# Kernel tuning notes

Hardware: AMD Instinct MI355X
Metric: run time of the kernel (lower is better)

The kernel has to match this reference:

```python
import jax, jax.numpy as jnp
import numpy as np

H = 1024
LENGTH = 48
N = 2048


def setup_inputs() -> dict:
    key = jax.random.key(0)
    k1, k2, k3, k4 = jax.random.split(key, 4)
    s = 1.0 / np.sqrt(H)  # torch LSTMCell init: U(-1/sqrt(H), 1/sqrt(H))
    h_in = jax.random.normal(k1, (N, H), dtype=jnp.float32)
    W_hh = jax.random.uniform(k2, (4 * H, H), minval=-s, maxval=s, dtype=jnp.float32)
    b_ih = jax.random.uniform(k3, (4 * H,), minval=-s, maxval=s, dtype=jnp.float32)
    b_hh = jax.random.uniform(k4, (4 * H,), minval=-s, maxval=s, dtype=jnp.float32)
    return {"h_in": h_in, "W_hh": W_hh, "b_ih": b_ih, "b_hh": b_hh}


def reference(h_in, W_hh, b_ih, b_hh):
    # LSTMCell with input_size=0: gates depend only on hidden state.
    # torch gate order: i, f, g, o.
    Hd = h_in.shape[1]
    bias = b_ih + b_hh
    c0 = jnp.zeros_like(h_in)

    def step(carry, _):
        h, c = carry
        z = h @ W_hh.T + bias  # (N, 4H)
        i = jax.nn.sigmoid(z[:, :Hd])
        f = jax.nn.sigmoid(z[:, Hd:2 * Hd])
        g = jnp.tanh(z[:, 2 * Hd:3 * Hd])
        o = jax.nn.sigmoid(z[:, 3 * Hd:])
        c_new = f * c + i * g
        h_new = o * jnp.tanh(c_new)
        return (h_new, c_new), h_new

    _, hs = jax.lax.scan(step, (h_in, c0), None, length=LENGTH)  # (L, N, H)
    return jnp.transpose(hs, (1, 2, 0))  # (N, H, L) matching torch.stack(axis=-1)
```

## Files before the change

kernel.cpp:

```cpp
#include <hip/hip_runtime.h>
#include <hip/hip_bf16.h>

#define Hdim 1024
#define Nb   2048
#define Lsteps 48

typedef unsigned short ushort_t;
typedef short bf16x8 __attribute__((ext_vector_type(8)));
typedef float f32x4 __attribute__((ext_vector_type(4)));

typedef __attribute__((address_space(3))) unsigned int lds_u32;
typedef const __attribute__((address_space(1))) unsigned int glb_u32;

__device__ __forceinline__ void gll16(const void* g, void* l) {
    __builtin_amdgcn_global_load_lds((glb_u32*)g, (lds_u32*)l, 16, 0, 0);
}

__device__ __forceinline__ ushort_t f2bf(float x) {
    unsigned u = __builtin_bit_cast(unsigned, x);
    unsigned r = u + 0x7fffu + ((u >> 16) & 1u);
    return (ushort_t)(r >> 16);
}

__device__ __forceinline__ float frcp(float x) { return __builtin_amdgcn_rcpf(x); }

__device__ __forceinline__ float fsigmoid(float x) {
    return frcp(1.0f + __expf(-x));
}
__device__ __forceinline__ float ftanh(float x) {
    float xm = fminf(fmaxf(x, -15.0f), 15.0f);
    float e = __expf(2.0f * xm);
    return (e - 1.0f) * frcp(e + 1.0f);
}

__device__ __forceinline__ f32x4 mfma16(bf16x8 a, bf16x8 b, f32x4 c) {
    return __builtin_amdgcn_mfma_f32_16x16x32_bf16(a, b, c, 0, 0, 0);
}

#define VMCNT8   asm volatile("s_waitcnt vmcnt(8)" ::: "memory")
#define VMCNT0   asm volatile("s_waitcnt vmcnt(0)" ::: "memory")
#define LGKMCNT0 asm volatile("s_waitcnt lgkmcnt(0)" ::: "memory")

__global__ __launch_bounds__(256) void prep_w(const float* __restrict__ W,
                                              ushort_t* __restrict__ Wb) {
    int i = blockIdx.x * 256 + threadIdx.x;
    Wb[i] = f2bf(W[i]);
}

__global__ __launch_bounds__(256) void prep_h(const float* __restrict__ h_in,
                                              ushort_t* __restrict__ h0,
                                              const float* __restrict__ b_ih,
                                              const float* __restrict__ b_hh,
                                              float* __restrict__ bias) {
    int i = blockIdx.x * 256 + threadIdx.x;
    h0[i] = f2bf(h_in[i]);
    if (i < 4 * Hdim) bias[i] = b_ih[i] + b_hh[i];
}

__global__ __launch_bounds__(256) void lstm_step(
    const ushort_t* __restrict__ hsrc,
    ushort_t* __restrict__ hdst,
    const ushort_t* __restrict__ Wb,
    const float* __restrict__ bias,
    float* __restrict__ cst,
    float* __restrict__ tmp)
{
    __shared__ __align__(16) ushort_t As[2][128 * 64];
    __shared__ __align__(16) ushort_t Bs[2][128 * 64];

    const int tid  = threadIdx.x;
    const int lane = tid & 63;
    const int wid  = tid >> 6;
    const int wr   = wid >> 1;
    const int wc   = wid & 1;

    const int p    = blockIdx.x;
    const int xcd  = p & 7;
    const int slot = p >> 3;
    const int jb   = (xcd >> 1) * 8 + (slot & 7);
    const int nb   = (xcd & 1) * 8 + (slot >> 3);
    const int n0   = nb * 128;
    const int j0   = jb * 32;

    f32x4 acc[4][4];
#pragma unroll
    for (int g = 0; g < 4; ++g)
#pragma unroll
        for (int ri = 0; ri < 4; ++ri)
            acc[g][ri] = (f32x4){0.f, 0.f, 0.f, 0.f};

    const int srow8  = lane >> 3;
    const int schunk = (lane & 7) ^ srow8;
    const int choff  = schunk * 8;

    const ushort_t* aGlob = hsrc + (size_t)(n0 + wid * 32 + srow8) * Hdim + choff;
    const ushort_t* bGlob = Wb + (size_t)(wid * Hdim + j0 + srow8) * Hdim + choff;

    const int lr   = lane & 15;
    const int rsw  = lr & 7;
    const int cq   = lane >> 4;

    auto STAGE = [&](int buf, int it) {
        const int k0 = it * 64;
#pragma unroll
        for (int ii = 0; ii < 4; ++ii)
            gll16(aGlob + (size_t)ii * 8 * Hdim + k0, &As[buf][(wid * 32 + ii * 8) * 64]);
#pragma unroll
        for (int ii = 0; ii < 4; ++ii)
            gll16(bGlob + (size_t)ii * 8 * Hdim + k0, &Bs[buf][(wid * 32 + ii * 8) * 64]);
    };

    auto COMPUTE = [&](int buf) {
#pragma unroll
        for (int kh = 0; kh < 2; ++kh) {
            const int ch = ((cq + kh * 4) ^ rsw) * 8;
            bf16x8 af[4], bfr[4];
#pragma unroll
            for (int ri = 0; ri < 4; ++ri) {
                int row = wr * 64 + ri * 16 + lr;
                af[ri] = *(const bf16x8*)&As[buf][row * 64 + ch];
            }
#pragma unroll
            for (int g = 0; g < 4; ++g) {
                int u = g * 32 + wc * 16 + lr;
                bfr[g] = *(const bf16x8*)&Bs[buf][u * 64 + ch];
            }
#pragma unroll
            for (int g = 0; g < 4; ++g)
#pragma unroll
                for (int ri = 0; ri < 4; ++ri)
                    acc[g][ri] = mfma16(af[ri], bfr[g], acc[g][ri]);
        }
    };

    STAGE(0, 0);
    STAGE(1, 1);
#pragma unroll 1
    for (int t = 0; t < 16; ++t) {
        const int cur = t & 1;
        if (t < 15) { VMCNT8; } else { VMCNT0; }
        __builtin_amdgcn_s_barrier();
        __builtin_amdgcn_s_setprio(1);
        COMPUTE(cur);
        __builtin_amdgcn_s_setprio(0);
        if (t < 15) {
            LGKMCNT0;
            __builtin_amdgcn_s_barrier();
            if (t < 14) STAGE(cur, t + 2);
        }
    }

    const int q4 = (lane >> 4) * 4;
    const int j  = j0 + wc * 16 + lr;
    const float bi = bias[j];
    const float bf = bias[Hdim + j];
    const float bg = bias[2 * Hdim + j];
    const float bo = bias[3 * Hdim + j];
#pragma unroll
    for (int ri = 0; ri < 4; ++ri)
#pragma unroll
        for (int q = 0; q < 4; ++q) {
            int n = n0 + wr * 64 + ri * 16 + q4 + q;
            float gi = fsigmoid(acc[0][ri][q] + bi);
            float gf = fsigmoid(acc[1][ri][q] + bf);
            float gg = ftanh(acc[2][ri][q] + bg);
            float go = fsigmoid(acc[3][ri][q] + bo);
            size_t idx = (size_t)n * Hdim + j;
            float cn = gf * cst[idx] + gi * gg;
            cst[idx] = cn;
            float hv = go * ftanh(cn);
            hdst[idx] = f2bf(hv);
            tmp[idx] = hv;
        }
}

__global__ __launch_bounds__(256) void flush16(const float* __restrict__ tmp,
                                               float* __restrict__ out, int t0) {
    int idx = blockIdx.x * 256 + threadIdx.x;
    float v[16];
#pragma unroll
    for (int s = 0; s < 16; ++s)
        v[s] = tmp[(size_t)s * (Nb * Hdim) + idx];
    float4* dst = (float4*)(out + (size_t)idx * Lsteps + t0);
#pragma unroll
    for (int s = 0; s < 4; ++s)
        dst[s] = make_float4(v[4 * s], v[4 * s + 1], v[4 * s + 2], v[4 * s + 3]);
}

extern "C" void kernel_launch(void* const* d_in, const int* in_sizes, int n_in,
                              void* d_out, int out_size, void* d_ws, size_t ws_size,
                              hipStream_t stream) {
    const float* h_in = (const float*)d_in[0];
    const float* W    = (const float*)d_in[1];
    const float* b_ih = (const float*)d_in[2];
    const float* b_hh = (const float*)d_in[3];
    float* out = (float*)d_out;

    char* ws = (char*)d_ws;
    ushort_t* Wb   = (ushort_t*)(ws);
    ushort_t* h0   = (ushort_t*)(ws + 8388608);
    ushort_t* h1   = (ushort_t*)(ws + 12582912);
    float*    cst  = (float*)(ws + 16777216);
    float*    bias = (float*)(ws + 25165824);
    float*    tmp16= (float*)(ws + 25182208);

    hipMemsetAsync(cst, 0, (size_t)Nb * Hdim * sizeof(float), stream);

    prep_w<<<(4 * Hdim * Hdim) / 256, 256, 0, stream>>>(W, Wb);
    prep_h<<<(Nb * Hdim) / 256, 256, 0, stream>>>(h_in, h0, b_ih, b_hh, bias);

    for (int t = 0; t < Lsteps; ++t) {
        const ushort_t* hs = (t & 1) ? h1 : h0;
        ushort_t*       hd = (t & 1) ? h0 : h1;
        float* tslot = tmp16 + (size_t)(t & 15) * (Nb * Hdim);
        lstm_step<<<512, 256, 0, stream>>>(hs, hd, Wb, bias, cst, tslot);
        if ((t & 15) == 15) {
            flush16<<<(Nb * Hdim) / 256, 256, 0, stream>>>(tmp16, out, t - 15);
        }
    }
}
```

Baseline: 1.724 ms.

## Enlarge LSTM step tile to 256 rows with 512 threads and triple buffering

Each step block now covers 256 batch rows and 128 gate columns using 8 waves, instead of 128 rows with 4 waves. The grid is halved to 256 blocks and the staging buffers move into dynamic shared memory. Global-to-LDS staging goes from double to triple buffering, with the vmcnt waits adjusted to match. The cell-state and bias reads are moved ahead of the GEMM loop to hide their latency. The larger tile reuses each weight tile across more rows and cuts redundant hidden-state loads. The cost is about 147KB of LDS per block, which limits occupancy to one block per CU, and fewer blocks to cover latency.

Result: slower. 1.784 ms (+3.4%).

```diff
diff --git a/kernel.cpp b/kernel.cpp
--- a/kernel.cpp
+++ b/kernel.cpp
@@ -4,6 +4,11 @@
 #define Hdim 1024
 #define Nb   2048
 #define Lsteps 48
+
+#define BM 256
+#define BROWS 128
+#define NT 16
+#define DEPTH 3
 
 typedef unsigned short ushort_t;
 typedef short bf16x8 __attribute__((ext_vector_type(8)));
@@ -23,10 +28,7 @@
 }
 
 __device__ __forceinline__ float frcp(float x) { return __builtin_amdgcn_rcpf(x); }
-
-__device__ __forceinline__ float fsigmoid(float x) {
-    return frcp(1.0f + __expf(-x));
-}
+__device__ __forceinline__ float fsigmoid(float x) { return frcp(1.0f + __expf(-x)); }
 __device__ __forceinline__ float ftanh(float x) {
     float xm = fminf(fmaxf(x, -15.0f), 15.0f);
     float e = __expf(2.0f * xm);
@@ -37,8 +39,9 @@
     return __builtin_amdgcn_mfma_f32_16x16x32_bf16(a, b, c, 0, 0, 0);
 }
 
-#define VMCNT8   asm volatile("s_waitcnt vmcnt(8)" ::: "memory")
-#define VMCNT0   asm volatile("s_waitcnt vmcnt(0)" ::: "memory")
+#define VMCNT12  asm volatile("s_waitcnt vmcnt(12)" ::: "memory")
+#define VMCNT6   asm volatile("s_waitcnt vmcnt(6)"  ::: "memory")
+#define VMCNT0   asm volatile("s_waitcnt vmcnt(0)"  ::: "memory")
 #define LGKMCNT0 asm volatile("s_waitcnt lgkmcnt(0)" ::: "memory")
 
 __global__ __launch_bounds__(256) void prep_w(const float* __restrict__ W,
@@ -57,7 +60,7 @@
     if (i < 4 * Hdim) bias[i] = b_ih[i] + b_hh[i];
 }
 
-__global__ __launch_bounds__(256) void lstm_step(
+__global__ __launch_bounds__(512, 2) void lstm_step(
     const ushort_t* __restrict__ hsrc,
     ushort_t* __restrict__ hdst,
     const ushort_t* __restrict__ Wb,
@@ -65,8 +68,9 @@
     float* __restrict__ cst,
     float* __restrict__ tmp)
 {
-    __shared__ __align__(16) ushort_t As[2][128 * 64];
-    __shared__ __align__(16) ushort_t Bs[2][128 * 64];
+    extern __shared__ __align__(16) ushort_t smem[];
+    ushort_t* As = smem;
+    ushort_t* Bs = smem + DEPTH * (BM * 64);
 
     const int tid  = threadIdx.x;
     const int lane = tid & 63;
@@ -78,9 +82,24 @@
     const int xcd  = p & 7;
     const int slot = p >> 3;
     const int jb   = (xcd >> 1) * 8 + (slot & 7);
-    const int nb   = (xcd & 1) * 8 + (slot >> 3);
-    const int n0   = nb * 128;
+    const int nb   = (xcd & 1) * 4 + (slot >> 3);
+    const int n0   = nb * BM;
     const int j0   = jb * 32;
+
+    const int lr   = lane & 15;
+    const int q4   = (lane >> 4) * 4;
+    const int j    = j0 + wc * 16 + lr;
+
+    float cpre[16];
+#pragma unroll
+    for (int ri = 0; ri < 4; ++ri)
+#pragma unroll
+        for (int q = 0; q < 4; ++q)
+            cpre[ri * 4 + q] = cst[(size_t)(n0 + wr * 64 + ri * 16 + q4 + q) * Hdim + j];
+    const float bi = bias[j];
+    const float bf = bias[Hdim + j];
+    const float bg = bias[2 * Hdim + j];
+    const float bo = bias[3 * Hdim + j];
 
     f32x4 acc[4][4];
 #pragma unroll
@@ -94,9 +113,8 @@
     const int choff  = schunk * 8;
 
     const ushort_t* aGlob = hsrc + (size_t)(n0 + wid * 32 + srow8) * Hdim + choff;
-    const ushort_t* bGlob = Wb + (size_t)(wid * Hdim + j0 + srow8) * Hdim + choff;
-
-    const int lr   = lane & 15;
+    const ushort_t* bGlob = Wb + (size_t)((wid >> 1) * Hdim + j0 + (wid & 1) * 16 + srow8) * Hdim + choff;
+
     const int rsw  = lr & 7;
     const int cq   = lane >> 4;
 
@@ -104,10 +122,12 @@
         const int k0 = it * 64;
 #pragma unroll
         for (int ii = 0; ii < 4; ++ii)
-            gll16(aGlob + (size_t)ii * 8 * Hdim + k0, &As[buf][(wid * 32 + ii * 8) * 64]);
-#pragma unroll
-        for (int ii = 0; ii < 4; ++ii)
-            gll16(bGlob + (size_t)ii * 8 * Hdim + k0, &Bs[buf][(wid * 32 + ii * 8) * 64]);
+            gll16(aGlob + (size_t)ii * 8 * Hdim + k0,
+                  &As[buf * (BM * 64) + (wid * 32 + ii * 8) * 64]);
+#pragma unroll
+        for (int ii = 0; ii < 2; ++ii)
+            gll16(bGlob + (size_t)ii * 8 * Hdim + k0,
+                  &Bs[buf * (BROWS * 64) + (wid * 16 + ii * 8) * 64]);
     };
 
     auto COMPUTE = [&](int buf) {
@@ -118,12 +138,12 @@
 #pragma unroll
             for (int ri = 0; ri < 4; ++ri) {
                 int row = wr * 64 + ri * 16 + lr;
-                af[ri] = *(const bf16x8*)&As[buf][row * 64 + ch];
+                af[ri] = *(const bf16x8*)&As[buf * (BM * 64) + row * 64 + ch];
             }
 #pragma unroll
             for (int g = 0; g < 4; ++g) {
                 int u = g * 32 + wc * 16 + lr;
-                bfr[g] = *(const bf16x8*)&Bs[buf][u * 64 + ch];
+                bfr[g] = *(const bf16x8*)&Bs[buf * (BROWS * 64) + u * 64 + ch];
             }
 #pragma unroll
             for (int g = 0; g < 4; ++g)
@@ -133,29 +153,25 @@
         }
     };
 
-    STAGE(0, 0);
-    STAGE(1, 1);
+    STAGE(0, 0); STAGE(1, 1); STAGE(2, 2);
+    int cur = 0;
 #pragma unroll 1
-    for (int t = 0; t < 16; ++t) {
-        const int cur = t & 1;
-        if (t < 15) { VMCNT8; } else { VMCNT0; }
+    for (int t = 0; t < NT; ++t) {
+        if (t <= NT - 3)      { VMCNT12; }
+        else if (t == NT - 2) { VMCNT6;  }
+        else                  { VMCNT0;  }
         __builtin_amdgcn_s_barrier();
         __builtin_amdgcn_s_setprio(1);
         COMPUTE(cur);
         __builtin_amdgcn_s_setprio(0);
-        if (t < 15) {
+        if (t <= NT - 4) {
             LGKMCNT0;
             __builtin_amdgcn_s_barrier();
-            if (t < 14) STAGE(cur, t + 2);
-        }
+            STAGE(cur, t + 3);
+        }
+        cur = (cur == 2) ? 0 : cur + 1;
     }
 
-    const int q4 = (lane >> 4) * 4;
-    const int j  = j0 + wc * 16 + lr;
-    const float bi = bias[j];
-    const float bf = bias[Hdim + j];
-    const float bg = bias[2 * Hdim + j];
-    const float bo = bias[3 * Hdim + j];
 #pragma unroll
     for (int ri = 0; ri < 4; ++ri)
 #pragma unroll
@@ -166,7 +182,7 @@
             float gg = ftanh(acc[2][ri][q] + bg);
             float go = fsigmoid(acc[3][ri][q] + bo);
             size_t idx = (size_t)n * Hdim + j;
-            float cn = gf * cst[idx] + gi * gg;
+            float cn = gf * cpre[ri * 4 + q] + gi * gg;
             cst[idx] = cn;
             float hv = go * ftanh(cn);
             hdst[idx] = f2bf(hv);
@@ -204,6 +220,15 @@
     float*    bias = (float*)(ws + 25165824);
     float*    tmp16= (float*)(ws + 25182208);
 
+    static bool attr_done = false;
+    if (!attr_done) {
+        hipFuncSetAttribute((const void*)lstm_step,
+                            hipFuncAttributeMaxDynamicSharedMemorySize,
+                            DEPTH * (BM * 64 + BROWS * 64) * (int)sizeof(ushort_t));
+        attr_done = true;
+    }
+    const int smem_bytes = DEPTH * (BM * 64 + BROWS * 64) * (int)sizeof(ushort_t);
+
     hipMemsetAsync(cst, 0, (size_t)Nb * Hdim * sizeof(float), stream);
 
     prep_w<<<(4 * Hdim * Hdim) / 256, 256, 0, stream>>>(W, Wb);
@@ -213,7 +238,7 @@
         const ushort_t* hs = (t & 1) ? h1 : h0;
         ushort_t*       hd = (t & 1) ? h0 : h1;
         float* tslot = tmp16 + (size_t)(t & 15) * (Nb * Hdim);
-        lstm_step<<<512, 256, 0, stream>>>(hs, hd, Wb, bias, cst, tslot);
+        lstm_step<<<256, 512, smem_bytes, stream>>>(hs, hd, Wb, bias, cst, tslot);
         if ((t & 15) == 15) {
             flush16<<<(Nb * Hdim) / 256, 256, 0, stream>>>(tmp16, out, t - 15);
         }
```
